# Kernel tuning notes

Hardware: AMD Instinct MI355X
Metric: run time of the kernel (lower is better)

## Reference

```python
import jax, jax.numpy as jnp
import numpy as np

B, N, D, H = 4, 1024, 1024, 16
DH = D // H  # 64
FF = 4 * D   # 4096


def _layernorm(x, w, b, eps=1e-5):
    mu = jnp.mean(x, axis=-1, keepdims=True)
    var = jnp.var(x, axis=-1, keepdims=True)
    return (x - mu) * jax.lax.rsqrt(var + eps) * w + b


def setup_inputs() -> dict:
    key = jax.random.key(0)
    ks = jax.random.split(key, 8)
    s = 0.02
    return {
        "x": jax.random.normal(ks[0], (B, N, D), jnp.float32),
        "ln1_w": jnp.ones((D,), jnp.float32),
        "ln1_b": jnp.zeros((D,), jnp.float32),
        "qkv_w": jax.random.normal(ks[1], (3 * D, D), jnp.float32) * s,
        "qkv_b": jnp.zeros((3 * D,), jnp.float32),
        "proj_l_w": jax.random.normal(ks[2], (H, H), jnp.float32) * s,
        "proj_l_b": jnp.zeros((H,), jnp.float32),
        "proj_w_w": jax.random.normal(ks[3], (H, H), jnp.float32) * s,
        "proj_w_b": jnp.zeros((H,), jnp.float32),
        "out_w": jax.random.normal(ks[4], (D, D), jnp.float32) * s,
        "out_b": jnp.zeros((D,), jnp.float32),
        "gamma1": jnp.ones((D,), jnp.float32),
        "ln2_w": jnp.ones((D,), jnp.float32),
        "ln2_b": jnp.zeros((D,), jnp.float32),
        "fc1_w": jax.random.normal(ks[5], (FF, D), jnp.float32) * s,
        "fc1_b": jnp.zeros((FF,), jnp.float32),
        "fc2_w": jax.random.normal(ks[6], (D, FF), jnp.float32) * s,
        "fc2_b": jnp.zeros((D,), jnp.float32),
        "gamma2": jnp.ones((D,), jnp.float32),
    }


def reference(x, ln1_w, ln1_b, qkv_w, qkv_b, proj_l_w, proj_l_b, proj_w_w,
              proj_w_b, out_w, out_b, gamma1, ln2_w, ln2_b, fc1_w, fc1_b,
              fc2_w, fc2_b, gamma2):
    # ---- LayerScale(TalkingHeadAttention) branch ----
    h = _layernorm(x, ln1_w, ln1_b)
    qkv = h @ qkv_w.T + qkv_b                      # [B,N,3D]
    q, k, v = jnp.split(qkv, 3, axis=-1)
    # [B,N,D] -> [B,H,N,DH]
    reshape = lambda t: t.reshape(B, N, H, DH).transpose(0, 2, 1, 3)
    q, k, v = reshape(q), reshape(k), reshape(v)
    attn = jnp.einsum("bhid,bhjd->bhij", q, k) * (DH ** -0.5)
    # talking-heads mixing before softmax (Linear over head dim)
    attn = jnp.einsum("bhij,gh->bgij", attn, proj_l_w) + proj_l_b[None, :, None, None]
    attn = jax.nn.softmax(attn, axis=-1)
    # talking-heads mixing after softmax
    attn = jnp.einsum("bhij,gh->bgij", attn, proj_w_w) + proj_w_b[None, :, None, None]
    o = jnp.einsum("bhij,bhjd->bhid", attn, v)     # [B,H,N,DH]
    o = o.transpose(0, 2, 1, 3).reshape(B, N, D)
    o = o @ out_w.T + out_b
    x = x + gamma1 * o
    # ---- LayerScale(MLP) branch ----
    h = _layernorm(x, ln2_w, ln2_b)
    h = jax.nn.gelu(h @ fc1_w.T + fc1_b)
    h = h @ fc2_w.T + fc2_b
    return x + gamma2 * h
```

## Files before the change

kernel.cpp:

```cpp
#include <hip/hip_runtime.h>


typedef _Float16 f16x8 __attribute__((ext_vector_type(8)));
typedef _Float16 f16x4 __attribute__((ext_vector_type(4)));
typedef _Float16 f16x2 __attribute__((ext_vector_type(2)));
typedef float f32x4 __attribute__((ext_vector_type(4)));

#define B_ 4
#define N_ 1024
#define D_ 1024
#define H_ 16
#define DH_ 64
#define FF_ 4096
#define M_ (B_ * N_)

__device__ __forceinline__ float gelu_act(float x) {
  float z = 0.7978845608028654f * (x + 0.044715f * x * x * x);
  return x / (1.0f + __expf(-2.0f * z));
}

__device__ __forceinline__ void ld_lds16(const _Float16* g, _Float16* l) {
  __builtin_amdgcn_global_load_lds((const __attribute__((address_space(1))) void*)g,
                                   (__attribute__((address_space(3))) void*)l, 16, 0, 0);
}

__device__ __forceinline__ int swz8(int i) {
  return (((i >> 2) << 1) ^ (i & 3)) & 7;
}
__device__ __forceinline__ int lds_off(int p, int i, int j) {
  int ch = ((j >> 3) ^ swz8(i) ^ ((p >> 2) << 1)) & 7;
  return p * 1032 + i * 64 + (ch << 3) + (j & 7);
}

__global__ __launch_bounds__(256) void cast_f32_f16(const float* __restrict__ in,
                                                    _Float16* __restrict__ out, int n) {
  int i = (blockIdx.x * 256 + threadIdx.x) * 4;
  if (i >= n) return;
  float4 v = *(const float4*)(in + i);
  f16x4 o;
  o[0] = (_Float16)v.x; o[1] = (_Float16)v.y; o[2] = (_Float16)v.z; o[3] = (_Float16)v.w;
  *(f16x4*)(out + i) = o;
}

__global__ __launch_bounds__(256) void prep_w(const float* __restrict__ W1,
                                              const float* __restrict__ W2,
                                              _Float16* __restrict__ w1f,
                                              _Float16* __restrict__ w2f) {
  int t = threadIdx.x;
  w1f[t] = (_Float16)W1[t];
  w2f[t] = (_Float16)W2[t];
}

__global__ __launch_bounds__(256) void vsum_k(const _Float16* __restrict__ vt,
                                              const float* __restrict__ b2,
                                              float* __restrict__ bsum) {
  int g = blockIdx.x, b = blockIdx.y;
  int t = threadIdx.x;
  int d = t >> 2, seg = t & 3;
  const _Float16* row = vt + (size_t)((b * H_ + g) * DH_ + d) * N_ + seg * 256;
  float s = 0.f;
  #pragma unroll
  for (int k = 0; k < 32; k++) {
    f16x8 v = *(const f16x8*)(row + k * 8);
    #pragma unroll
    for (int e = 0; e < 8; e++) s += (float)v[e];
  }
  s += __shfl_xor(s, 1);
  s += __shfl_xor(s, 2);
  if (seg == 0) bsum[b * D_ + g * 64 + d] = b2[g] * s;
}

__global__ __launch_bounds__(256) void ln_f16(const float* __restrict__ x,
                                              const float* __restrict__ w,
                                              const float* __restrict__ b,
                                              _Float16* __restrict__ out) {
  int row = blockIdx.x;
  int tid = threadIdx.x;
  const float* xr = x + (size_t)row * D_;
  float4 v = *(const float4*)(xr + tid * 4);
  float s = v.x + v.y + v.z + v.w;
  float sq = v.x * v.x + v.y * v.y + v.z * v.z + v.w * v.w;
  #pragma unroll
  for (int off = 32; off > 0; off >>= 1) {
    s += __shfl_down(s, off);
    sq += __shfl_down(sq, off);
  }
  __shared__ float red[8];
  int wave = tid >> 6, lane = tid & 63;
  if (lane == 0) { red[wave] = s; red[4 + wave] = sq; }
  __syncthreads();
  float ts = red[0] + red[1] + red[2] + red[3];
  float tq = red[4] + red[5] + red[6] + red[7];
  float mean = ts * (1.0f / (float)D_);
  float var = tq * (1.0f / (float)D_) - mean * mean;
  float rs = rsqrtf(var + 1e-5f);
  float4 wv = *(const float4*)(w + tid * 4);
  float4 bv = *(const float4*)(b + tid * 4);
  f16x4 o;
  o[0] = (_Float16)((v.x - mean) * rs * wv.x + bv.x);
  o[1] = (_Float16)((v.y - mean) * rs * wv.y + bv.y);
  o[2] = (_Float16)((v.z - mean) * rs * wv.z + bv.z);
  o[3] = (_Float16)((v.w - mean) * rs * wv.w + bv.w);
  *(f16x4*)(out + (size_t)row * D_ + tid * 4) = o;
}

template <int EPI, int BN, int OCC>
__global__ __launch_bounds__(256, OCC) void gemm_nt(
    const _Float16* __restrict__ A, const _Float16* __restrict__ W,
    const float* __restrict__ bias, int M, int N, int K,
    _Float16* __restrict__ outB, float* __restrict__ outF,
    const float* __restrict__ res, const float* __restrict__ gamma) {
  __shared__ _Float16 As[128 * 64];
  __shared__ _Float16 Bs[BN * 64];
  int tid = threadIdx.x;
  int wave = tid >> 6, lane = tid & 63;
  int quad = lane >> 4, l16 = lane & 15;
  int wm = wave >> 1, wn = wave & 1;
  int m0 = blockIdx.y * 128, n0 = blockIdx.x * BN;
  int lrow = lane >> 3, lcol = (lane & 7) * 8;
  const int NI = (BN == 128) ? 4 : 2;
  const int WN = (BN == 128) ? 64 : 32;

  f32x4 zero = {0.f, 0.f, 0.f, 0.f};
  f32x4 acc[4][NI];
  #pragma unroll
  for (int i = 0; i < 4; i++)
    #pragma unroll
    for (int j = 0; j < NI; j++) acc[i][j] = zero;

  for (int k0 = 0; k0 < K; k0 += 64) {
    __syncthreads();
    #pragma unroll
    for (int c = 0; c < 4; c++) {
      int rb = c * 32 + wave * 8;
      ld_lds16(A + (size_t)(m0 + rb + lrow) * K + k0 + lcol, As + rb * 64);
      if (BN == 128 || c < 2)
        ld_lds16(W + (size_t)(n0 + rb + lrow) * K + k0 + lcol, Bs + rb * 64);
    }
    __syncthreads();
    #pragma unroll
    for (int ks = 0; ks < 2; ks++) {
      int kk = ks * 32 + quad * 8;
      f16x8 a[4], bfr[NI];
      #pragma unroll
      for (int i = 0; i < 4; i++) a[i] = *(const f16x8*)(As + (wm * 64 + i * 16 + l16) * 64 + kk);
      #pragma unroll
      for (int i = 0; i < NI; i++) bfr[i] = *(const f16x8*)(Bs + (wn * WN + i * 16 + l16) * 64 + kk);
      #pragma unroll
      for (int mi = 0; mi < 4; mi++)
        #pragma unroll
        for (int ni = 0; ni < NI; ni++)
          acc[mi][ni] = __builtin_amdgcn_mfma_f32_16x16x32_f16(a[mi], bfr[ni], acc[mi][ni], 0, 0, 0);
    }
  }

  #pragma unroll
  for (int mi = 0; mi < 4; mi++) {
    int grow_base = m0 + wm * 64 + mi * 16 + quad * 4;
    #pragma unroll
    for (int ni = 0; ni < NI; ni++) {
      int gcol = n0 + wn * WN + ni * 16 + l16;
      float bb = bias[gcol];
      float gm = (EPI == 1) ? gamma[gcol] : 0.f;
      #pragma unroll
      for (int r = 0; r < 4; r++) {
        size_t oi = (size_t)(grow_base + r) * N + gcol;
        float c = acc[mi][ni][r] + bb;
        if (EPI == 0) {
          outB[oi] = (_Float16)c;
        } else if (EPI == 1) {
          outF[oi] = res[oi] + gm * c;
        } else {
          outB[oi] = (_Float16)gelu_act(c);
        }
      }
    }
  }
}

__global__ __launch_bounds__(256) void transpose_v(const _Float16* __restrict__ qkv,
                                                   _Float16* __restrict__ vt) {
  int jt = blockIdx.x;
  int h = blockIdx.y;
  int b = blockIdx.z;
  __shared__ _Float16 tl[64][68];
  int tid = threadIdx.x;
  int j0 = jt * 64;
  #pragma unroll
  for (int k = 0; k < 16; k++) {
    int idx = k * 256 + tid;
    int jr = idx >> 6, dc = idx & 63;
    tl[jr][dc] = qkv[(size_t)(b * N_ + j0 + jr) * (3 * D_) + 2 * D_ + h * 64 + dc];
  }
  __syncthreads();
  #pragma unroll
  for (int k = 0; k < 16; k++) {
    int idx = k * 256 + tid;
    int dr = idx >> 6, jc = idx & 63;
    vt[(size_t)((b * H_ + h) * DH_ + dr) * N_ + j0 + jc] = tl[jc][dr];
  }
}

__global__ __launch_bounds__(1024, 4) void attn_th(
    const _Float16* __restrict__ qkv, const _Float16* __restrict__ vt,
    const _Float16* __restrict__ w1f, const _Float16* __restrict__ w2f,
    const float* __restrict__ b1f, const float* __restrict__ bsum,
    _Float16* __restrict__ ob) {
  __shared__ __align__(16) _Float16 SP[2 * 16512];
  __shared__ float lsum[272];
  _Float16* Sp = SP;
  _Float16* Pp = SP + 16512;

  const int tid = threadIdx.x;
  const int wave = tid >> 6;
  const int lane = tid & 63;
  const int quad = lane >> 4, l16 = lane & 15;
  const int i0 = blockIdx.x * 16;
  const int b = blockIdx.y;
  const size_t bN = (size_t)b * N_;
  const f32x4 zero = {0.f, 0.f, 0.f, 0.f};

  f16x8 qf[2];
  #pragma unroll
  for (int ks = 0; ks < 2; ks++) {
    f16x8 q = *(const f16x8*)(qkv + (bN + i0 + l16) * 3072 + wave * 64 + ks * 32 + quad * 8);
    #pragma unroll
    for (int e = 0; e < 8; e++) q[e] = q[e] * (_Float16)0.125f;
    qf[ks] = q;
  }
  f16x4 w1a = *(const f16x4*)(w1f + l16 * 16 + quad * 4);
  float b1v = b1f[l16];
  f32x4 b1i = {b1v, b1v, b1v, b1v};

  const _Float16* vbase = vt + (size_t)((b * H_ + wave) * DH_ + l16) * N_ + quad * 8;

  f32x4 uacc[4];
  #pragma unroll
  for (int nt = 0; nt < 4; nt++) uacc[nt] = zero;
  float lacc = 0.f;

  f16x8 kcur[4][2];
  auto loadK = [&](int j0) {
    #pragma unroll
    for (int jb = 0; jb < 4; jb++) {
      const _Float16* kb = qkv + (bN + j0 + jb * 16 + l16) * 3072 + 1024 + wave * 64 + quad * 8;
      kcur[jb][0] = *(const f16x8*)kb;
      kcur[jb][1] = *(const f16x8*)(kb + 32);
    }
  };
  loadK(0);

  f16x8 vreg[4];

  for (int t = 0; t < 16; t++) {
    int j0 = t * 64;
    f32x4 sres[4];
    #pragma unroll
    for (int jb = 0; jb < 4; jb++) {
      f32x4 s = __builtin_amdgcn_mfma_f32_16x16x32_f16(kcur[jb][0], qf[0], zero, 0, 0, 0);
      sres[jb] = __builtin_amdgcn_mfma_f32_16x16x32_f16(kcur[jb][1], qf[1], s, 0, 0, 0);
    }
    #pragma unroll
    for (int jb = 0; jb < 4; jb++) {
      f16x4 sv;
      #pragma unroll
      for (int r = 0; r < 4; r++) sv[r] = (_Float16)sres[jb][r];
      *(f16x4*)(Sp + lds_off(wave, l16, jb * 16 + quad * 4)) = sv;
    }
    if (t < 15) loadK(j0 + 64);
    #pragma unroll
    for (int nt = 0; nt < 4; nt++)
      vreg[nt] = *(const f16x8*)(vbase + (size_t)(nt * 16) * N_ + j0);
    __syncthreads();
    #pragma unroll
    for (int cg = 0; cg < 4; cg++) {
      f16x4 sf;
      #pragma unroll
      for (int t4 = 0; t4 < 4; t4++)
        sf[t4] = Sp[lds_off(quad * 4 + t4, wave, cg * 16 + l16)];
      f32x4 a = __builtin_amdgcn_mfma_f32_16x16x16f16(sf, w1a, b1i, 0, 0, 0);
      f16x4 pv;
      #pragma unroll
      for (int r = 0; r < 4; r++) {
        float e = __expf(a[r]);
        lacc += e;
        pv[r] = (_Float16)e;
      }
      *(f16x4*)(Pp + lds_off(l16, wave, cg * 16 + quad * 4)) = pv;
    }
    __syncthreads();
    f16x8 pf0 = *(const f16x8*)(Pp + lds_off(wave, l16, quad * 8));
    f16x8 pf1 = *(const f16x8*)(Pp + lds_off(wave, l16, 32 + quad * 8));
    #pragma unroll
    for (int nt = 0; nt < 4; nt++)
      uacc[nt] = __builtin_amdgcn_mfma_f32_16x16x32_f16(vreg[nt], pf0, uacc[nt], 0, 0, 0);
    #pragma unroll
    for (int nt = 0; nt < 4; nt++) {
      f16x8 vf = *(const f16x8*)(vbase + (size_t)(nt * 16) * N_ + j0 + 32);
      uacc[nt] = __builtin_amdgcn_mfma_f32_16x16x32_f16(vf, pf1, uacc[nt], 0, 0, 0);
    }
  }

  lacc += __shfl_xor(lacc, 16);
  lacc += __shfl_xor(lacc, 32);
  __syncthreads();
  if (quad == 0) lsum[l16 * 17 + wave] = lacc;
  __syncthreads();
  float invl = 1.0f / lsum[wave * 17 + l16];

  _Float16* Uf = Sp;
  #pragma unroll
  for (int nt = 0; nt < 4; nt++) {
    f16x4 u;
    #pragma unroll
    for (int r = 0; r < 4; r++) u[r] = (_Float16)(uacc[nt][r] * invl);
    *(f16x4*)(Uf + wave * 1092 + l16 * 68 + nt * 16 + quad * 4) = u;
  }
  __syncthreads();

  f16x4 w2a = *(const f16x4*)(w2f + l16 * 16 + quad * 4);
  #pragma unroll
  for (int cg = 0; cg < 4; cg++) {
    f16x4 af;
    #pragma unroll
    for (int t4 = 0; t4 < 4; t4++)
      af[t4] = Uf[(quad * 4 + t4) * 1092 + wave * 68 + cg * 16 + l16];
    f32x4 o = __builtin_amdgcn_mfma_f32_16x16x16f16(af, w2a, zero, 0, 0, 0);
    f32x4 bs = *(const f32x4*)(bsum + b * D_ + l16 * 64 + cg * 16 + quad * 4);
    f16x4 ov;
    #pragma unroll
    for (int r = 0; r < 4; r++) ov[r] = (_Float16)(o[r] + bs[r]);
    *(f16x4*)(ob + (bN + i0 + wave) * D_ + l16 * 64 + cg * 16 + quad * 4) = ov;
  }
}

extern "C" void kernel_launch(void* const* d_in, const int* in_sizes, int n_in,
                              void* d_out, int out_size, void* d_ws, size_t ws_size,
                              hipStream_t stream) {
  const float* x      = (const float*)d_in[0];
  const float* ln1_w  = (const float*)d_in[1];
  const float* ln1_b  = (const float*)d_in[2];
  const float* qkv_w  = (const float*)d_in[3];
  const float* qkv_b  = (const float*)d_in[4];
  const float* plw    = (const float*)d_in[5];
  const float* plb    = (const float*)d_in[6];
  const float* pww    = (const float*)d_in[7];
  const float* pwb    = (const float*)d_in[8];
  const float* out_w  = (const float*)d_in[9];
  const float* out_b  = (const float*)d_in[10];
  const float* gamma1 = (const float*)d_in[11];
  const float* ln2_w  = (const float*)d_in[12];
  const float* ln2_b  = (const float*)d_in[13];
  const float* fc1_w  = (const float*)d_in[14];
  const float* fc1_b  = (const float*)d_in[15];
  const float* fc2_w  = (const float*)d_in[16];
  const float* fc2_b  = (const float*)d_in[17];
  const float* gamma2 = (const float*)d_in[18];
  float* out = (float*)d_out;

  char* ws = (char*)d_ws;
  _Float16* wq   = (_Float16*)(ws + 0);
  _Float16* wo   = (_Float16*)(ws + 6291456);
  _Float16* wf1  = (_Float16*)(ws + 8388608);
  _Float16* wf2  = (_Float16*)(ws + 16777216);
  float*    x1   = (float*)   (ws + 25165824);
  _Float16* ob   = (_Float16*)(ws + 41943040);
  _Float16* hb   = (_Float16*)(ws + 50331648);
  _Float16* qkvb = (_Float16*)(ws + 58720256);
  _Float16* vtb  = (_Float16*)(ws + 83886080);
  _Float16* fb   = (_Float16*)(ws + 58720256);
  _Float16* w1f  = (_Float16*)(ws + 8388608);
  _Float16* w2f  = (_Float16*)(ws + 8388608 + 512);
  float*    bsum = (float*)   (ws + 8388608 + 1024);
  if (ws_size < 92274688) return;

  cast_f32_f16<<<3072 * 1024 / 1024, 256, 0, stream>>>(qkv_w, wq, 3072 * 1024);
  cast_f32_f16<<<1024 * 1024 / 1024, 256, 0, stream>>>(out_w, wo, 1024 * 1024);
  prep_w<<<1, 256, 0, stream>>>(plw, pww, w1f, w2f);

  ln_f16<<<4096, 256, 0, stream>>>(x, ln1_w, ln1_b, hb);
  gemm_nt<0, 128, 3><<<dim3(24, 32), 256, 0, stream>>>(hb, wq, qkv_b, M_, 3 * D_, D_, qkvb, nullptr, nullptr, nullptr);
  transpose_v<<<dim3(16, 16, 4), 256, 0, stream>>>(qkvb, vtb);
  vsum_k<<<dim3(16, 4), 256, 0, stream>>>(vtb, pwb, bsum);
  attn_th<<<dim3(64, 4), 1024, 0, stream>>>(qkvb, vtb, w1f, w2f, plb, bsum, ob);
  gemm_nt<1, 64, 4><<<dim3(16, 32), 256, 0, stream>>>(ob, wo, out_b, M_, D_, D_, nullptr, x1, x, gamma1);

  cast_f32_f16<<<4096 * 1024 / 1024, 256, 0, stream>>>(fc1_w, wf1, 4096 * 1024);
  cast_f32_f16<<<4096 * 1024 / 1024, 256, 0, stream>>>(fc2_w, wf2, 4096 * 1024);

  ln_f16<<<4096, 256, 0, stream>>>(x1, ln2_w, ln2_b, hb);
  gemm_nt<2, 128, 3><<<dim3(32, 32), 256, 0, stream>>>(hb, wf1, fc1_b, M_, FF_, D_, fb, nullptr, nullptr, nullptr);
  gemm_nt<1, 64, 4><<<dim3(16, 32), 256, 0, stream>>>(fb, wf2, fc2_b, M_, D_, FF_, nullptr, out, x1, gamma2);
}
```

Measured before the change: 479.4 us.

## Split attention over key halves, add reduction kernel, fuse V-sum into transpose

```diff
diff --git a/kernel.cpp b/kernel.cpp
--- a/kernel.cpp
+++ b/kernel.cpp
@@ -3,7 +3,6 @@
 
 typedef _Float16 f16x8 __attribute__((ext_vector_type(8)));
 typedef _Float16 f16x4 __attribute__((ext_vector_type(4)));
-typedef _Float16 f16x2 __attribute__((ext_vector_type(2)));
 typedef float f32x4 __attribute__((ext_vector_type(4)));
 
 #define B_ 4
@@ -45,29 +44,13 @@
 __global__ __launch_bounds__(256) void prep_w(const float* __restrict__ W1,
                                               const float* __restrict__ W2,
                                               _Float16* __restrict__ w1f,
-                                              _Float16* __restrict__ w2f) {
+                                              _Float16* __restrict__ w2f,
+                                              float* __restrict__ bsum) {
   int t = threadIdx.x;
   w1f[t] = (_Float16)W1[t];
   w2f[t] = (_Float16)W2[t];
-}
-
-__global__ __launch_bounds__(256) void vsum_k(const _Float16* __restrict__ vt,
-                                              const float* __restrict__ b2,
-                                              float* __restrict__ bsum) {
-  int g = blockIdx.x, b = blockIdx.y;
-  int t = threadIdx.x;
-  int d = t >> 2, seg = t & 3;
-  const _Float16* row = vt + (size_t)((b * H_ + g) * DH_ + d) * N_ + seg * 256;
-  float s = 0.f;
-  #pragma unroll
-  for (int k = 0; k < 32; k++) {
-    f16x8 v = *(const f16x8*)(row + k * 8);
-    #pragma unroll
-    for (int e = 0; e < 8; e++) s += (float)v[e];
-  }
-  s += __shfl_xor(s, 1);
-  s += __shfl_xor(s, 2);
-  if (seg == 0) bsum[b * D_ + g * 64 + d] = b2[g] * s;
+  #pragma unroll
+  for (int k = 0; k < 16; k++) bsum[t * 16 + k] = 0.f;
 }
 
 __global__ __launch_bounds__(256) void ln_f16(const float* __restrict__ x,
@@ -104,29 +87,27 @@
   *(f16x4*)(out + (size_t)row * D_ + tid * 4) = o;
 }
 
-template <int EPI, int BN, int OCC>
-__global__ __launch_bounds__(256, OCC) void gemm_nt(
+template <int EPI>
+__global__ __launch_bounds__(256, 3) void gemm_nt(
     const _Float16* __restrict__ A, const _Float16* __restrict__ W,
     const float* __restrict__ bias, int M, int N, int K,
     _Float16* __restrict__ outB, float* __restrict__ outF,
     const float* __restrict__ res, const float* __restrict__ gamma) {
   __shared__ _Float16 As[128 * 64];
-  __shared__ _Float16 Bs[BN * 64];
+  __shared__ _Float16 Bs[128 * 64];
   int tid = threadIdx.x;
   int wave = tid >> 6, lane = tid & 63;
   int quad = lane >> 4, l16 = lane & 15;
   int wm = wave >> 1, wn = wave & 1;
-  int m0 = blockIdx.y * 128, n0 = blockIdx.x * BN;
+  int m0 = blockIdx.y * 128, n0 = blockIdx.x * 128;
   int lrow = lane >> 3, lcol = (lane & 7) * 8;
-  const int NI = (BN == 128) ? 4 : 2;
-  const int WN = (BN == 128) ? 64 : 32;
 
   f32x4 zero = {0.f, 0.f, 0.f, 0.f};
-  f32x4 acc[4][NI];
+  f32x4 acc[4][4];
   #pragma unroll
   for (int i = 0; i < 4; i++)
     #pragma unroll
-    for (int j = 0; j < NI; j++) acc[i][j] = zero;
+    for (int j = 0; j < 4; j++) acc[i][j] = zero;
 
   for (int k0 = 0; k0 < K; k0 += 64) {
     __syncthreads();
@@ -134,22 +115,21 @@
     for (int c = 0; c < 4; c++) {
       int rb = c * 32 + wave * 8;
       ld_lds16(A + (size_t)(m0 + rb + lrow) * K + k0 + lcol, As + rb * 64);
-      if (BN == 128 || c < 2)
-        ld_lds16(W + (size_t)(n0 + rb + lrow) * K + k0 + lcol, Bs + rb * 64);
+      ld_lds16(W + (size_t)(n0 + rb + lrow) * K + k0 + lcol, Bs + rb * 64);
     }
     __syncthreads();
     #pragma unroll
     for (int ks = 0; ks < 2; ks++) {
       int kk = ks * 32 + quad * 8;
-      f16x8 a[4], bfr[NI];
+      f16x8 a[4], bfr[4];
       #pragma unroll
       for (int i = 0; i < 4; i++) a[i] = *(const f16x8*)(As + (wm * 64 + i * 16 + l16) * 64 + kk);
       #pragma unroll
-      for (int i = 0; i < NI; i++) bfr[i] = *(const f16x8*)(Bs + (wn * WN + i * 16 + l16) * 64 + kk);
+      for (int i = 0; i < 4; i++) bfr[i] = *(const f16x8*)(Bs + (wn * 64 + i * 16 + l16) * 64 + kk);
       #pragma unroll
       for (int mi = 0; mi < 4; mi++)
         #pragma unroll
-        for (int ni = 0; ni < NI; ni++)
+        for (int ni = 0; ni < 4; ni++)
           acc[mi][ni] = __builtin_amdgcn_mfma_f32_16x16x32_f16(a[mi], bfr[ni], acc[mi][ni], 0, 0, 0);
     }
   }
@@ -158,8 +138,8 @@
   for (int mi = 0; mi < 4; mi++) {
     int grow_base = m0 + wm * 64 + mi * 16 + quad * 4;
     #pragma unroll
-    for (int ni = 0; ni < NI; ni++) {
-      int gcol = n0 + wn * WN + ni * 16 + l16;
+    for (int ni = 0; ni < 4; ni++) {
+      int gcol = n0 + wn * 64 + ni * 16 + l16;
       float bb = bias[gcol];
       float gm = (EPI == 1) ? gamma[gcol] : 0.f;
       #pragma unroll
@@ -178,8 +158,10 @@
   }
 }
 
-__global__ __launch_bounds__(256) void transpose_v(const _Float16* __restrict__ qkv,
-                                                   _Float16* __restrict__ vt) {
+__global__ __launch_bounds__(256) void transpose_vsum(const _Float16* __restrict__ qkv,
+                                                      const float* __restrict__ b2,
+                                                      _Float16* __restrict__ vt,
+                                                      float* __restrict__ bsum) {
   int jt = blockIdx.x;
   int h = blockIdx.y;
   int b = blockIdx.z;
@@ -199,15 +181,18 @@
     int dr = idx >> 6, jc = idx & 63;
     vt[(size_t)((b * H_ + h) * DH_ + dr) * N_ + j0 + jc] = tl[jc][dr];
   }
-}
-
-__global__ __launch_bounds__(1024, 4) void attn_th(
+  int d = tid & 63, ch = tid >> 6;
+  float s = 0.f;
+  #pragma unroll
+  for (int k = 0; k < 16; k++) s += (float)tl[ch * 16 + k][d];
+  atomicAdd(bsum + b * D_ + h * 64 + d, b2[h] * s);
+}
+
+__global__ __launch_bounds__(1024, 8) void attn_th(
     const _Float16* __restrict__ qkv, const _Float16* __restrict__ vt,
-    const _Float16* __restrict__ w1f, const _Float16* __restrict__ w2f,
-    const float* __restrict__ b1f, const float* __restrict__ bsum,
-    _Float16* __restrict__ ob) {
+    const _Float16* __restrict__ w1f, const float* __restrict__ b1f,
+    _Float16* __restrict__ upart, float* __restrict__ lpart) {
   __shared__ __align__(16) _Float16 SP[2 * 16512];
-  __shared__ float lsum[272];
   _Float16* Sp = SP;
   _Float16* Pp = SP + 16512;
 
@@ -215,8 +200,10 @@
   const int wave = tid >> 6;
   const int lane = tid & 63;
   const int quad = lane >> 4, l16 = lane & 15;
-  const int i0 = blockIdx.x * 16;
-  const int b = blockIdx.y;
+  const int it = blockIdx.x;
+  const int jh = blockIdx.y;
+  const int b = blockIdx.z;
+  const int i0 = it * 16;
   const size_t bN = (size_t)b * N_;
   const f32x4 zero = {0.f, 0.f, 0.f, 0.f};
 
@@ -248,12 +235,13 @@
       kcur[jb][1] = *(const f16x8*)(kb + 32);
     }
   };
-  loadK(0);
+  const int jbase = jh * 512;
+  loadK(jbase);
 
   f16x8 vreg[4];
 
-  for (int t = 0; t < 16; t++) {
-    int j0 = t * 64;
+  for (int t = 0; t < 8; t++) {
+    int j0 = jbase + t * 64;
     f32x4 sres[4];
     #pragma unroll
     for (int jb = 0; jb < 4; jb++) {
@@ -267,7 +255,7 @@
       for (int r = 0; r < 4; r++) sv[r] = (_Float16)sres[jb][r];
       *(f16x4*)(Sp + lds_off(wave, l16, jb * 16 + quad * 4)) = sv;
     }
-    if (t < 15) loadK(j0 + 64);
+    if (t < 7) loadK(j0 + 64);
     #pragma unroll
     for (int nt = 0; nt < 4; nt++)
       vreg[nt] = *(const f16x8*)(vbase + (size_t)(nt * 16) * N_ + j0);
@@ -303,34 +291,62 @@
 
   lacc += __shfl_xor(lacc, 16);
   lacc += __shfl_xor(lacc, 32);
-  __syncthreads();
-  if (quad == 0) lsum[l16 * 17 + wave] = lacc;
-  __syncthreads();
-  float invl = 1.0f / lsum[wave * 17 + l16];
-
-  _Float16* Uf = Sp;
+  const size_t bi = ((size_t)(b * 64 + it)) * 2 + jh;
+  if (quad == 0) lpart[bi * 256 + l16 * 16 + wave] = lacc;
   #pragma unroll
   for (int nt = 0; nt < 4; nt++) {
     f16x4 u;
     #pragma unroll
-    for (int r = 0; r < 4; r++) u[r] = (_Float16)(uacc[nt][r] * invl);
-    *(f16x4*)(Uf + wave * 1092 + l16 * 68 + nt * 16 + quad * 4) = u;
-  }
+    for (int r = 0; r < 4; r++) u[r] = (_Float16)uacc[nt][r];
+    *(f16x4*)(upart + bi * 16384 + wave * 1024 + l16 * 64 + nt * 16 + quad * 4) = u;
+  }
+}
+
+__global__ __launch_bounds__(1024, 2) void attn_red(
+    const _Float16* __restrict__ upart, const float* __restrict__ lpart,
+    const _Float16* __restrict__ w2f, const float* __restrict__ bsum,
+    _Float16* __restrict__ ob) {
+  __shared__ __align__(16) _Float16 Uf[18560];
+  const int tid = threadIdx.x;
+  const int it = blockIdx.x;
+  const int b = blockIdx.y;
+  const size_t bi0 = ((size_t)(b * 64 + it)) * 2;
+
+  int e = tid >> 6, ii = (tid >> 2) & 15, d0 = (tid & 3) * 16;
+  float l = lpart[bi0 * 256 + e * 16 + ii] + lpart[(bi0 + 1) * 256 + e * 16 + ii];
+  float invl = 1.0f / l;
+  const _Float16* u0 = upart + bi0 * 16384 + tid * 16;
+  const _Float16* u1 = u0 + 16384;
+  f16x8 x0 = *(const f16x8*)u0, x1 = *(const f16x8*)(u0 + 8);
+  f16x8 y0 = *(const f16x8*)u1, y1 = *(const f16x8*)(u1 + 8);
+  f16x8 o0, o1;
+  #pragma unroll
+  for (int k = 0; k < 8; k++) {
+    o0[k] = (_Float16)(((float)x0[k] + (float)y0[k]) * invl);
+    o1[k] = (_Float16)(((float)x1[k] + (float)y1[k]) * invl);
+  }
+  _Float16* dst = Uf + e * 1160 + ii * 72 + d0;
+  *(f16x8*)dst = o0;
+  *(f16x8*)(dst + 8) = o1;
   __syncthreads();
 
+  const int wave = tid >> 6, lane = tid & 63;
+  const int quad = lane >> 4, l16 = lane & 15;
+  const f32x4 zero = {0.f, 0.f, 0.f, 0.f};
+  const size_t bN = (size_t)b * N_;
   f16x4 w2a = *(const f16x4*)(w2f + l16 * 16 + quad * 4);
   #pragma unroll
   for (int cg = 0; cg < 4; cg++) {
     f16x4 af;
     #pragma unroll
     for (int t4 = 0; t4 < 4; t4++)
-      af[t4] = Uf[(quad * 4 + t4) * 1092 + wave * 68 + cg * 16 + l16];
+      af[t4] = Uf[(quad * 4 + t4) * 1160 + wave * 72 + cg * 16 + l16];
     f32x4 o = __builtin_amdgcn_mfma_f32_16x16x16f16(af, w2a, zero, 0, 0, 0);
     f32x4 bs = *(const f32x4*)(bsum + b * D_ + l16 * 64 + cg * 16 + quad * 4);
     f16x4 ov;
     #pragma unroll
     for (int r = 0; r < 4; r++) ov[r] = (_Float16)(o[r] + bs[r]);
-    *(f16x4*)(ob + (bN + i0 + wave) * D_ + l16 * 64 + cg * 16 + quad * 4) = ov;
+    *(f16x4*)(ob + (bN + it * 16 + wave) * D_ + l16 * 64 + cg * 16 + quad * 4) = ov;
   }
 }
 
@@ -372,23 +388,25 @@
   _Float16* w1f  = (_Float16*)(ws + 8388608);
   _Float16* w2f  = (_Float16*)(ws + 8388608 + 512);
   float*    bsum = (float*)   (ws + 8388608 + 1024);
+  float*    lpart = (float*)   (ws + 0);
+  _Float16* upart = (_Float16*)(ws + 25165824);
   if (ws_size < 92274688) return;
 
   cast_f32_f16<<<3072 * 1024 / 1024, 256, 0, stream>>>(qkv_w, wq, 3072 * 1024);
   cast_f32_f16<<<1024 * 1024 / 1024, 256, 0, stream>>>(out_w, wo, 1024 * 1024);
-  prep_w<<<1, 256, 0, stream>>>(plw, pww, w1f, w2f);
+  prep_w<<<1, 256, 0, stream>>>(plw, pww, w1f, w2f, bsum);
 
   ln_f16<<<4096, 256, 0, stream>>>(x, ln1_w, ln1_b, hb);
-  gemm_nt<0, 128, 3><<<dim3(24, 32), 256, 0, stream>>>(hb, wq, qkv_b, M_, 3 * D_, D_, qkvb, nullptr, nullptr, nullptr);
-  transpose_v<<<dim3(16, 16, 4), 256, 0, stream>>>(qkvb, vtb);
-  vsum_k<<<dim3(16, 4), 256, 0, stream>>>(vtb, pwb, bsum);
-  attn_th<<<dim3(64, 4), 1024, 0, stream>>>(qkvb, vtb, w1f, w2f, plb, bsum, ob);
-  gemm_nt<1, 64, 4><<<dim3(16, 32), 256, 0, stream>>>(ob, wo, out_b, M_, D_, D_, nullptr, x1, x, gamma1);
+  gemm_nt<0><<<dim3(24, 32), 256, 0, stream>>>(hb, wq, qkv_b, M_, 3 * D_, D_, qkvb, nullptr, nullptr, nullptr);
+  transpose_vsum<<<dim3(16, 16, 4), 256, 0, stream>>>(qkvb, pwb, vtb, bsum);
+  attn_th<<<dim3(64, 2, 4), 1024, 0, stream>>>(qkvb, vtb, w1f, plb, upart, lpart);
+  attn_red<<<dim3(64, 4), 1024, 0, stream>>>(upart, lpart, w2f, bsum, ob);
+  gemm_nt<1><<<dim3(8, 32), 256, 0, stream>>>(ob, wo, out_b, M_, D_, D_, nullptr, x1, x, gamma1);
 
   cast_f32_f16<<<4096 * 1024 / 1024, 256, 0, stream>>>(fc1_w, wf1, 4096 * 1024);
   cast_f32_f16<<<4096 * 1024 / 1024, 256, 0, stream>>>(fc2_w, wf2, 4096 * 1024);
 
   ln_f16<<<4096, 256, 0, stream>>>(x1, ln2_w, ln2_b, hb);
-  gemm_nt<2, 128, 3><<<dim3(32, 32), 256, 0, stream>>>(hb, wf1, fc1_b, M_, FF_, D_, fb, nullptr, nullptr, nullptr);
-  gemm_nt<1, 64, 4><<<dim3(16, 32), 256, 0, stream>>>(fb, wf2, fc2_b, M_, D_, FF_, nullptr, out, x1, gamma2);
-}
+  gemm_nt<2><<<dim3(32, 32), 256, 0, stream>>>(hb, wf1, fc1_b, M_, FF_, D_, fb, nullptr, nullptr, nullptr);
+  gemm_nt<1><<<dim3(8, 32), 256, 0, stream>>>(fb, wf2, fc2_b, M_, D_, FF_, nullptr, out, x1, gamma2);
+}
```

Result: slower. 670.4 us (+39.9%).
